# Kernel optimization log

Hardware: AMD Instinct MI355X
Metric: run time of the kernel (lower is better)

## Reference

```python
import jax, jax.numpy as jnp
import numpy as np

WS = 8
SHIFT = 4


def _cpb_constants(ws):
    rc = np.arange(-(ws - 1), ws, dtype=np.float32)
    gh, gw = np.meshgrid(rc, rc, indexing='ij')
    table = np.stack([gh, gw], axis=-1)[None]  # (1, 2ws-1, 2ws-1, 2)
    table = table / (ws - 1) * 8.0
    table = np.sign(table) * np.log2(np.abs(table) + 1.0) / np.log2(8.0)
    c = np.arange(ws)
    ch, cw = np.meshgrid(c, c, indexing='ij')
    flat = np.stack([ch.ravel(), cw.ravel()])  # (2, N)
    rel = (flat[:, :, None] - flat[:, None, :]).transpose(1, 2, 0).copy()
    rel[..., 0] += ws - 1
    rel[..., 1] += ws - 1
    rel[..., 0] *= 2 * ws - 1
    rpi = rel.sum(-1)  # (N, N) int
    return table.astype(np.float32), rpi


def _attn_mask(H, W, ws, s):
    # Faithful to source: middle slice is slice(-ws, +s) (empty for H>ws+s)
    img = np.zeros((H, W), np.float32)
    cnt = 0
    for hs in (slice(0, -ws), slice(-ws, s), slice(-s, None)):
        for wsl in (slice(0, -ws), slice(-ws, s), slice(-s, None)):
            img[hs, wsl] = cnt
            cnt += 1
    mw = img.reshape(H // ws, ws, W // ws, ws).transpose(0, 2, 1, 3).reshape(-1, ws * ws)
    am = mw[:, None, :] - mw[:, :, None]
    return np.where(am != 0, -100.0, 0.0).astype(np.float32)


def _dwconv(x, w):
    return jax.lax.conv_general_dilated(
        x, w, (1, 1), 'SAME',
        dimension_numbers=('NCHW', 'OIHW', 'NCHW'),
        feature_group_count=x.shape[1])


def _ln_nchw(x, g, b, eps=8e-8):
    m = x.mean(1, keepdims=True)
    v = jnp.square(x - m).mean(1, keepdims=True)
    return (x - m) / jnp.sqrt(v + eps) * g[None, :, None, None] + b[None, :, None, None]


def setup_inputs() -> dict:
    key = jax.random.key(0)
    ks = jax.random.split(key, 16)
    B, C, H, W = 16, 512, 64, 64
    nh = 16
    hid = 4 * C
    w = lambda k, s: (jax.random.normal(k, s, dtype=jnp.float32) * 0.02)
    return {
        'x': jax.random.normal(ks[0], (B, C, H, W), dtype=jnp.float32),
        'lpu_w': w(ks[1], (C, 1, 3, 3)),
        'qkv_w': w(ks[2], (3 * C, C)),
        'out_w': w(ks[3], (C, C)),
        'cpb_w1': w(ks[4], (512, 2)),
        'cpb_w2': w(ks[5], (nh, 512)),
        'logits_scale': jnp.full((nh, 1, 1), np.log(10.0), dtype=jnp.float32),
        'gamma1': jnp.ones((C,), jnp.float32),
        'beta1': jnp.zeros((C,), jnp.float32),
        'gamma2': jnp.ones((C,), jnp.float32),
        'beta2': jnp.zeros((C,), jnp.float32),
        'pw1_w': w(ks[6], (hid, C)),
        'dw_w': w(ks[7], (hid, 1, 3, 3)),
        'pw2_w': w(ks[8], (C, hid)),
        'sr_scale': jnp.ones((), jnp.float32),
        'sr_bias': jnp.zeros((), jnp.float32),
        'rs1': jnp.ones((C,), jnp.float32),
        'rs2': jnp.ones((C,), jnp.float32),
    }


def reference(x, lpu_w, qkv_w, out_w, cpb_w1, cpb_w2, logits_scale,
              gamma1, beta1, gamma2, beta2, pw1_w, dw_w, pw2_w,
              sr_scale, sr_bias, rs1, rs2):
    B, C, H, W = x.shape
    ws, s = WS, SHIFT
    nh = logits_scale.shape[0]
    hd = C // nh
    N = ws * ws
    table_np, rpi = _cpb_constants(ws)
    table = jnp.asarray(table_np)
    mask = jnp.asarray(_attn_mask(H, W, ws, s))  # (nW, N, N)

    # LPU: x + depthwise conv
    x = x + _dwconv(x, lpu_w)
    x_temp = x

    # flatten to (B, HW, C); faithful roll over dims (1,2) = tokens AND channels
    x = x.reshape(B, C, H * W).transpose(0, 2, 1)
    x = jnp.roll(x, (-s, -s), axis=(1, 2))
    # window partition
    x = x.reshape(B, H // ws, ws, W // ws, ws, C).transpose(0, 1, 3, 2, 4, 5).reshape(-1, N, C)
    Bw = x.shape[0]

    qkv = (x @ qkv_w.T).reshape(Bw, N, 3, nh, hd).transpose(2, 0, 3, 1, 4)
    q, k, v = qkv[0], qkv[1], qkv[2]
    qn = q / jnp.maximum(jnp.linalg.norm(q, axis=-1, keepdims=True), 1e-12)
    kn = k / jnp.maximum(jnp.linalg.norm(k, axis=-1, keepdims=True), 1e-12)
    scale = jnp.exp(jnp.minimum(logits_scale, jnp.log(jnp.float32(100.0))))
    attn = jnp.einsum('bhid,bhjd->bhij', qn, kn) * scale[None]

    # continuous position bias
    tbl = jax.nn.hard_swish(table @ cpb_w1.T) @ cpb_w2.T  # (1, 2ws-1, 2ws-1, nh)
    tbl = tbl.reshape(-1, nh)
    bias = tbl[rpi.reshape(-1)].reshape(N, N, nh).transpose(2, 0, 1)
    bias = 16.0 * jax.nn.sigmoid(bias)
    attn = attn + bias[None]

    nW = mask.shape[0]
    attn = (attn.reshape(Bw // nW, nW, nh, N, N) + mask[None, :, None]).reshape(-1, nh, N, N)
    # faithful: nn.Softmax(1) -> softmax over HEAD axis
    attn = jax.nn.softmax(attn, axis=1)

    o = jnp.einsum('bhij,bhjd->bhid', attn, v).transpose(0, 2, 1, 3).reshape(Bw, N, C)
    o = o @ out_w.T

    o = o.reshape(B, H // ws, ws, W // ws, ws, C)
    o = jnp.roll(o, (s, s), axis=(1, 2))  # faithful: rolls window-grid / row dims
    # faithful buggy un-partition: transpose(1,2) then reshape
    o = o.transpose(0, 2, 1, 3, 4, 5).reshape(B, C, H, W)

    x = rs1[None, :, None, None] * x_temp + _ln_nchw(o, gamma1, beta1)

    h = jnp.einsum('bchw,oc->bohw', x, pw1_w)
    h = h + _dwconv(h, dw_w)
    h = sr_scale * jnp.square(jax.nn.relu(h)) + sr_bias  # StarReLU
    y = jnp.einsum('bchw,oc->bohw', h, pw2_w)
    return rs2[None, :, None, None] * x + _ln_nchw(y, gamma2, beta2)
```

## Files before the change

kernel.cpp:

```cpp
#include <hip/hip_runtime.h>
#include <hip/hip_bf16.h>
#include <stdint.h>


typedef float f32x4 __attribute__((ext_vector_type(4)));
typedef short s16x8 __attribute__((ext_vector_type(8)));

__device__ __forceinline__ float b2f(short u) {
  return __uint_as_float(((unsigned)(unsigned short)u) << 16);
}
__device__ __forceinline__ short f2b(float f) {
  __hip_bfloat16 h = __float2bfloat16(f);
  short s;
  __builtin_memcpy(&s, &h, 2);
  return s;
}
__device__ __forceinline__ void gload16(const void* g, void* l) {
  __builtin_amdgcn_global_load_lds((const unsigned int*)g, (unsigned int*)l, 16, 0, 0);
}

__global__ __launch_bounds__(256) void k_f2b4(const float* __restrict__ s0, short* __restrict__ d0,
                                              const float* __restrict__ s1, short* __restrict__ d1,
                                              const float* __restrict__ s2, short* __restrict__ d2,
                                              const float* __restrict__ s3, short* __restrict__ d3) {
  int b = blockIdx.x;
  const float* s;
  short* d;
  int base;
  if (b < 768) { s = s0; d = d0; base = b * 1024; }
  else if (b < 1024) { s = s1; d = d1; base = (b - 768) * 1024; }
  else if (b < 2048) { s = s2; d = d2; base = (b - 1024) * 1024; }
  else { s = s3; d = d3; base = (b - 2048) * 1024; }
  int i = base + threadIdx.x * 4;
  f32x4 v = *(const f32x4*)&s[i];
  ushort4 o;
  o.x = (unsigned short)f2b(v[0]);
  o.y = (unsigned short)f2b(v[1]);
  o.z = (unsigned short)f2b(v[2]);
  o.w = (unsigned short)f2b(v[3]);
  *(ushort4*)&d[i] = o;
}

__global__ __launch_bounds__(64) void k_cpb(const float* __restrict__ w1,
                                            const float* __restrict__ w2,
                                            float* __restrict__ btab) {
  const int r = blockIdx.x;
  const int lane = threadIdx.x;
  const int ri = r / 15, rj = r % 15;
  float th = (float)(ri - 7) * (8.f / 7.f);
  float tw = (float)(rj - 7) * (8.f / 7.f);
  float gh = copysignf(log2f(fabsf(th) + 1.f) * (1.f / 3.f), th);
  float gw = copysignf(log2f(fabsf(tw) + 1.f) * (1.f / 3.f), tw);
  const int h = lane >> 2, pp = lane & 3;
  float acc = 0.f;
  for (int k = 0; k < 128; ++k) {
    int hh = pp * 128 + k;
    float a = gh * w1[hh * 2] + gw * w1[hh * 2 + 1];
    float r6 = fminf(fmaxf(a + 3.f, 0.f), 6.f);
    float hsw = a * r6 * (1.f / 6.f);
    acc += hsw * w2[h * 512 + hh];
  }
  acc += __shfl_xor(acc, 1);
  acc += __shfl_xor(acc, 2);
  if ((lane & 3) == 0) btab[h * 225 + r] = 16.f / (1.f + __expf(-acc));
}

__global__ __launch_bounds__(256) void k_lpu(const float* __restrict__ x,
                                             const float* __restrict__ lw,
                                             short* __restrict__ xt) {
  __shared__ float img[64 * 68];
  const int bc = blockIdx.x;
  const int c = bc & 511;
  const float* img_g = x + (size_t)bc * 4096;
  short* outp = xt + (size_t)bc * 4096;
  const int tid = threadIdx.x;
#pragma unroll
  for (int t = 0; t < 4; ++t) {
    int idx = t * 256 + tid;
    int h = idx >> 4, w4 = (idx & 15) * 4;
    f32x4 v = *(const f32x4*)&img_g[h * 64 + w4];
    *(f32x4*)&img[h * 68 + w4] = v;
  }
  float wreg[9];
#pragma unroll
  for (int t = 0; t < 9; ++t) wreg[t] = lw[c * 9 + t];
  __syncthreads();
  const int hb = tid >> 4, w0 = (tid & 15) * 4;
#pragma unroll
  for (int g = 0; g < 4; ++g) {
    int h = hb + g * 16;
    float row[3][6];
#pragma unroll
    for (int dr = 0; dr < 3; ++dr) {
      int hh = h - 1 + dr;
      if (hh < 0 || hh > 63) {
#pragma unroll
        for (int j = 0; j < 6; ++j) row[dr][j] = 0.f;
      } else {
        f32x4 m = *(const f32x4*)&img[hh * 68 + w0];
        row[dr][1] = m[0]; row[dr][2] = m[1]; row[dr][3] = m[2]; row[dr][4] = m[3];
        row[dr][0] = (w0 > 0) ? img[hh * 68 + w0 - 1] : 0.f;
        row[dr][5] = (w0 < 60) ? img[hh * 68 + w0 + 4] : 0.f;
      }
    }
    ushort4 o;
    unsigned short op[4];
#pragma unroll
    for (int p = 0; p < 4; ++p) {
      float acc = row[1][p + 1];
#pragma unroll
      for (int dr = 0; dr < 3; ++dr)
#pragma unroll
        for (int dc = 0; dc < 3; ++dc)
          acc += wreg[dr * 3 + dc] * row[dr][p + dc];
      op[p] = (unsigned short)f2b(acc);
    }
    o.x = op[0]; o.y = op[1]; o.z = op[2]; o.w = op[3];
    *(ushort4*)&outp[h * 64 + w0] = o;
  }
}

__global__ __launch_bounds__(256) void k_xpose(const short* __restrict__ xt,
                                               short* __restrict__ xw) {
  __shared__ short tile[64][132];
  const int tid = threadIdx.x;
  const int cq = blockIdx.x & 3;
  const int h = (blockIdx.x >> 2) & 63;
  const int b = blockIdx.x >> 8;
  const int c0 = cq * 128;
  for (int idx = tid; idx < 64 * 128; idx += 256) {
    int ww = idx & 63, cc = idx >> 6;
    int csrc = (c0 + cc + 4) & 511;
    tile[ww][cc] = xt[(((size_t)b * 512 + csrc) * 64 + h) * 64 + ww];
  }
  __syncthreads();
  for (int qd = tid; qd < 64 * 32; qd += 256) {
    int ws_ = qd >> 5, cqq = qd & 31, cc = cqq * 4;
    int t = (h * 64 + ws_ + 4092) & 4095;
    int hd = t >> 6, wd = t & 63;
    int tok = (b * 64 + (hd >> 3) * 8 + (wd >> 3)) * 64 + (hd & 7) * 8 + (wd & 7);
    ushort4 u = *(const ushort4*)&tile[ws_][cc];
    *(ushort4*)&xw[(size_t)tok * 512 + c0 + cc] = u;
  }
}

template <int EPI>
__global__ __launch_bounds__(512, 2) void k_gemm(const short* __restrict__ A,
                                                 const short* __restrict__ B,
                                                 short* __restrict__ C,
                                                 short* __restrict__ o4,
                                                 const float* __restrict__ lsc,
                                                 int N, int K, int gx) {
  __shared__ short smem[2 * 32768];
  const int nwg = gridDim.x;
  const int orig = blockIdx.x;
  const int wgid = (orig & 7) * (nwg >> 3) + (orig >> 3);
  const int bx = wgid % gx, by = wgid / gx;
  const int tid = threadIdx.x;
  const int lane = tid & 63, wid = tid >> 6;
  const int wm = wid >> 2, wn = wid & 3;
  const int m0 = by * 256, n0 = bx * 256;
  const f32x4 fz = {0.f, 0.f, 0.f, 0.f};
  f32x4 acc[8][4];
#pragma unroll
  for (int m = 0; m < 8; ++m)
#pragma unroll
    for (int n = 0; n < 4; ++n) acc[m][n] = fz;
  const int rst = lane >> 3;
  const int cst = ((lane & 7) ^ rst) * 8;
  const int l15 = lane & 15, l4 = lane >> 4, l7 = lane & 7;
  const short* ag[4];
  const short* bg[4];
#pragma unroll
  for (int l = 0; l < 4; ++l) {
    int r = wid * 32 + l * 8 + rst;
    ag[l] = A + (size_t)(m0 + r) * K + cst;
    bg[l] = B + (size_t)(n0 + r) * K + cst;
  }
  const int nt = K >> 6;
  auto STAGE = [&](int b) {
    short* as = smem + b * 32768;
    short* bs = as + 16384;
#pragma unroll
    for (int l = 0; l < 4; ++l) {
      int rb = wid * 32 + l * 8;
      gload16(ag[l], as + rb * 64);
      gload16(bg[l], bs + rb * 64);
      ag[l] += 64;
      bg[l] += 64;
    }
  };
  STAGE(0);
  for (int kt = 0; kt < nt; ++kt) {
    const int cur = kt & 1;
    if (kt + 1 < nt) {
      STAGE(cur ^ 1);
      asm volatile("s_waitcnt vmcnt(8)" ::: "memory");
    } else {
      asm volatile("s_waitcnt vmcnt(0)" ::: "memory");
    }
    __builtin_amdgcn_s_barrier();
    __builtin_amdgcn_sched_barrier(0);
    const short* as = smem + cur * 32768;
    const short* bs = as + 16384;
    __builtin_amdgcn_s_setprio(1);
#pragma unroll
    for (int ks = 0; ks < 2; ++ks) {
      const int slot = ((ks * 4 + l4) ^ l7) * 8;
      s16x8 bfr[4];
#pragma unroll
      for (int n = 0; n < 4; ++n)
        bfr[n] = *(const s16x8*)&bs[(wn * 64 + n * 16 + l15) * 64 + slot];
#pragma unroll
      for (int m = 0; m < 8; ++m) {
        s16x8 af = *(const s16x8*)&as[(wm * 128 + m * 16 + l15) * 64 + slot];
#pragma unroll
        for (int n = 0; n < 4; ++n)
          acc[m][n] = __builtin_amdgcn_mfma_f32_16x16x32_bf16(af, bfr[n],
                                                              acc[m][n], 0, 0, 0);
      }
    }
    __builtin_amdgcn_s_setprio(0);
    __builtin_amdgcn_sched_barrier(0);
    __builtin_amdgcn_s_barrier();
    __builtin_amdgcn_sched_barrier(0);
  }
  if (EPI == 2) {
#pragma unroll
    for (int b = 0; b < 2; ++b) {
      const int cb = n0 + wn * 64 + b * 32;
      if (cb < 1024) {
        float sc = 1.f;
        if (cb < 512) sc = __expf(fminf(lsc[cb >> 5], 4.605170185988092f));
#pragma unroll
        for (int m = 0; m < 8; ++m)
#pragma unroll
          for (int r = 0; r < 4; ++r) {
            float s0 = acc[m][2 * b][r], s1 = acc[m][2 * b + 1][r];
            float ss = s0 * s0 + s1 * s1;
            ss += __shfl_xor(ss, 1);
            ss += __shfl_xor(ss, 2);
            ss += __shfl_xor(ss, 4);
            ss += __shfl_xor(ss, 8);
            float mul = sc / fmaxf(sqrtf(ss), 1e-12f);
            acc[m][2 * b][r] = s0 * mul;
            acc[m][2 * b + 1][r] = s1 * mul;
          }
      }
    }
  }
  short* ct = smem;
#pragma unroll
  for (int p = 0; p < 2; ++p) {
    if (p) __syncthreads();
    if (wm == p) {
#pragma unroll
      for (int m = 0; m < 8; ++m)
#pragma unroll
        for (int n = 0; n < 4; ++n)
#pragma unroll
          for (int r = 0; r < 4; ++r) {
            int lr = m * 16 + l4 * 4 + r;
            int lc = (wn * 64 + n * 16 + l15) ^ (((lr >> 2) & 3) << 4);
            ct[lr * 272 + lc] = f2b(acc[m][n][r]);
          }
    }
    __syncthreads();
#pragma unroll
    for (int uu = 0; uu < 8; ++uu) {
      int unit = uu * 512 + tid;
      int lr = unit >> 5, sl = unit & 31;
      int sx = (sl * 8) ^ (((lr >> 2) & 3) << 4);
      s16x8 v = *(const s16x8*)&ct[lr * 272 + sx];
      int grow = m0 + p * 128 + lr;
      int gcol = n0 + sl * 8;
      if (EPI != 1) {
        *(s16x8*)&C[(size_t)grow * N + gcol] = v;
      } else {
        int win = grow >> 6, nn = grow & 63;
        int b = win >> 6, whs = (win >> 3) & 7, wws = win & 7;
        int ih = nn >> 3, iw = nn & 7;
        int wh = (whs + 4) & 7, ww = (wws + 4) & 7;
        int cp = ww * 64 + wh * 8 + ih;
        int hp = iw * 8 + (gcol >> 6);
        int wp = gcol & 63;
        *(s16x8*)&o4[(((size_t)b * 512 + cp) * 64 + hp) * 64 + wp] = v;
      }
    }
  }
}

__global__ __launch_bounds__(256) void k_attn(const short* __restrict__ qkv,
                                              const float* __restrict__ btab_g,
                                              short* __restrict__ o_ws) {
  __shared__ float btab[3600];
  __shared__ short vts[2][2048];
  __shared__ short pts[4][1024];
  const int tid = threadIdx.x, lane = tid & 63, wid = tid >> 6;
  const int win = blockIdx.x;
  const int l15 = lane & 15, l4 = lane >> 4;
  const int qrow0 = wid * 16;
  for (int i = tid; i < 3600; i += 256) btab[i] = btab_g[i];
  int baddr[4][4];
#pragma unroll
  for (int n = 0; n < 4; ++n)
#pragma unroll
    for (int r = 0; r < 4; ++r) {
      int i_ = qrow0 + l4 * 4 + r, j_ = n * 16 + l15;
      int dih = (i_ >> 3) - (j_ >> 3) + 7;
      int diw = (i_ & 7) - (j_ & 7) + 7;
      baddr[n][r] = dih * 15 + diw;
    }
  __syncthreads();
  const short* base = qkv + (size_t)win * 64 * 1536;
  const f32x4 fz = {0.f, 0.f, 0.f, 0.f};
  f32x4 sump[4] = {fz, fz, fz, fz};
#pragma unroll 2
  for (int h = 0; h < 16; ++h) {
    s16x8 qf = *(const s16x8*)(base + (size_t)(qrow0 + l15) * 1536 + h * 32 + l4 * 8);
#pragma unroll
    for (int n = 0; n < 4; ++n) {
      s16x8 kf = *(const s16x8*)(base + (size_t)(n * 16 + l15) * 1536 + 512 + h * 32 + l4 * 8);
      f32x4 s = __builtin_amdgcn_mfma_f32_16x16x32_bf16(qf, kf, fz, 0, 0, 0);
#pragma unroll
      for (int r = 0; r < 4; ++r)
        sump[n][r] += __expf(s[r] + btab[h * 225 + baddr[n][r]]);
    }
  }
  f32x4 rden[4];
#pragma unroll
  for (int n = 0; n < 4; ++n)
#pragma unroll
    for (int r = 0; r < 4; ++r) rden[n][r] = 1.f / sump[n][r];
  char* pt = (char*)pts[wid];
  {
    int j = tid & 63, d0 = (tid >> 6) * 8;
    s16x8 vv = *(const s16x8*)(base + (size_t)j * 1536 + 1024 + d0);
#pragma unroll
    for (int jj = 0; jj < 8; ++jj) {
      int d = d0 + jj;
      *(short*)((char*)vts[0] + ((d * 128 + j * 2) ^ ((d & 7) << 4))) = vv[jj];
    }
  }
  __syncthreads();
  for (int h = 0; h < 16; ++h) {
    const char* vcur = (const char*)vts[h & 1];
    if (h < 15) {
      int j = tid & 63, d0 = (tid >> 6) * 8;
      s16x8 vv = *(const s16x8*)(base + (size_t)j * 1536 + 1024 + (h + 1) * 32 + d0);
      char* vnxt = (char*)vts[(h + 1) & 1];
#pragma unroll
      for (int jj = 0; jj < 8; ++jj) {
        int d = d0 + jj;
        *(short*)(vnxt + ((d * 128 + j * 2) ^ ((d & 7) << 4))) = vv[jj];
      }
    }
    s16x8 qf = *(const s16x8*)(base + (size_t)(qrow0 + l15) * 1536 + h * 32 + l4 * 8);
#pragma unroll
    for (int n = 0; n < 4; ++n) {
      s16x8 kf = *(const s16x8*)(base + (size_t)(n * 16 + l15) * 1536 + 512 + h * 32 + l4 * 8);
      f32x4 s = __builtin_amdgcn_mfma_f32_16x16x32_bf16(qf, kf, fz, 0, 0, 0);
#pragma unroll
      for (int r = 0; r < 4; ++r) {
        float pv = __expf(s[r] + btab[h * 225 + baddr[n][r]]) * rden[n][r];
        int i_loc = l4 * 4 + r, j_ = n * 16 + l15;
        *(short*)(pt + ((i_loc * 128 + j_ * 2) ^ ((i_loc & 7) << 4))) = f2b(pv);
      }
    }
    f32x4 oacc[2] = {fz, fz};
#pragma unroll
    for (int kb = 0; kb < 2; ++kb) {
      s16x8 af = *(const s16x8*)(pt + ((l15 * 128 + kb * 64 + l4 * 16) ^ ((l15 & 7) << 4)));
#pragma unroll
      for (int db = 0; db < 2; ++db) {
        int d = db * 16 + l15;
        s16x8 bf = *(const s16x8*)(vcur + ((d * 128 + kb * 64 + l4 * 16) ^ ((d & 7) << 4)));
        oacc[db] = __builtin_amdgcn_mfma_f32_16x16x32_bf16(af, bf, oacc[db], 0, 0, 0);
      }
    }
    short* ob = o_ws + ((size_t)win * 64 + qrow0) * 512 + h * 32;
#pragma unroll
    for (int db = 0; db < 2; ++db)
#pragma unroll
      for (int r = 0; r < 4; ++r)
        ob[(size_t)(l4 * 4 + r) * 512 + db * 16 + l15] = f2b(oacc[db][r]);
    __syncthreads();
  }
}

__global__ __launch_bounds__(256) void k_ln1(const short* __restrict__ o4,
                                             const short* __restrict__ xt,
                                             const float* __restrict__ g1,
                                             const float* __restrict__ b1,
                                             const float* __restrict__ rs1,
                                             short* __restrict__ x2h) {
  __shared__ float reds[4][64], redq[4][64];
  __shared__ float mean_s[64], rstd_s[64];
  __shared__ short tile[128][66];
  const int tid = threadIdx.x;
  const int b = blockIdx.x >> 6, hp = blockIdx.x & 63;
  const int w = tid & 63, part = tid >> 6;
  const short* base = o4 + (size_t)b * 512 * 4096 + hp * 64;
  float s = 0.f, q = 0.f;
  for (int c = part; c < 512; c += 4) {
    float v = b2f(base[(size_t)c * 4096 + w]);
    s += v; q += v * v;
  }
  reds[part][w] = s; redq[part][w] = q;
  __syncthreads();
  if (tid < 64) {
    float S = 0.f, Q = 0.f;
    for (int i = 0; i < 4; ++i) { S += reds[i][tid]; Q += redq[i][tid]; }
    float m = S * (1.f / 512.f);
    float var = Q * (1.f / 512.f) - m * m;
    mean_s[tid] = m;
    rstd_s[tid] = rsqrtf(var + 8e-8f);
  }
  __syncthreads();
  const short* xtb = xt + (size_t)b * 512 * 4096 + hp * 64;
  for (int c0 = 0; c0 < 512; c0 += 128) {
    for (int cc = part; cc < 128; cc += 4) {
      int c = c0 + cc;
      float v = b2f(base[(size_t)c * 4096 + w]);
      float ln = (v - mean_s[w]) * rstd_s[w] * g1[c] + b1[c];
      float xv = rs1[c] * b2f(xtb[(size_t)c * 4096 + w]) + ln;
      tile[cc][w] = f2b(xv);
    }
    __syncthreads();
    short* xh = x2h + ((size_t)blockIdx.x * 64) * 512 + c0;
    for (int qd = tid; qd < 64 * 32; qd += 256) {
      int w_ = qd >> 5, cq = qd & 31, cc = cq * 4;
      ushort4 u;
      u.x = (unsigned short)tile[cc][w_];
      u.y = (unsigned short)tile[cc + 1][w_];
      u.z = (unsigned short)tile[cc + 2][w_];
      u.w = (unsigned short)tile[cc + 3][w_];
      *(ushort4*)&xh[(size_t)w_ * 512 + cc] = u;
    }
    __syncthreads();
  }
}

__global__ __launch_bounds__(256) void k_dwc2(const short* __restrict__ h1,
                                              const float* __restrict__ dw,
                                              const float* __restrict__ srs_p,
                                              const float* __restrict__ srb_p,
                                              short* __restrict__ h2) {
  __shared__ short tile[6 * 64 * 64];
  const int tid = threadIdx.x;
  const int cblk = blockIdx.x & 31;
  const int hq = (blockIdx.x >> 5) & 15;
  const int b = blockIdx.x >> 9;
  const int c0 = cblk * 64;
  const int h0 = hq * 4;
  for (int t = 0; t < 12; ++t) {
    int idx = t * 256 + tid;
    int cg = idx & 7;
    int wl = (idx >> 3) & 63;
    int rl = idx >> 9;
    int hr = h0 - 1 + rl;
    s16x8 v = {0, 0, 0, 0, 0, 0, 0, 0};
    if (hr >= 0 && hr < 64)
      v = *(const s16x8*)&h1[((size_t)b * 4096 + hr * 64 + wl) * 2048 + c0 + cg * 8];
    *(s16x8*)&tile[(rl * 64 + wl) * 64 + (cg ^ (wl & 7)) * 8] = v;
  }
  const int cg = tid & 7;
  const int wq = tid >> 3;
  float wt[9][8];
#pragma unroll
  for (int j = 0; j < 8; ++j) {
    int cch = c0 + cg * 8 + j;
#pragma unroll
    for (int t = 0; t < 9; ++t) wt[t][j] = dw[cch * 9 + t];
  }
  const float srs = *srs_p, srb = *srb_p;
  __syncthreads();
#pragma unroll
  for (int it = 0; it < 8; ++it) {
    int wl = wq + (it & 1) * 32;
    int rl = it >> 1;
    s16x8 ctr = *(const s16x8*)&tile[((rl + 1) * 64 + wl) * 64 + (cg ^ (wl & 7)) * 8];
    float acc[8];
#pragma unroll
    for (int j = 0; j < 8; ++j) acc[j] = b2f(ctr[j]);
#pragma unroll
    for (int dh = -1; dh <= 1; ++dh) {
      int row = rl + 1 + dh;
#pragma unroll
      for (int dwi = -1; dwi <= 1; ++dwi) {
        int wn = wl + dwi;
        if (wn < 0 || wn > 63) continue;
        s16x8 v = *(const s16x8*)&tile[(row * 64 + wn) * 64 + (cg ^ (wn & 7)) * 8];
        const float* wrow = wt[(dh + 1) * 3 + dwi + 1];
#pragma unroll
        for (int j = 0; j < 8; ++j) acc[j] += wrow[j] * b2f(v[j]);
      }
    }
    s16x8 o;
#pragma unroll
    for (int j = 0; j < 8; ++j) {
      float rr = fmaxf(acc[j], 0.f);
      o[j] = f2b(srs * rr * rr + srb);
    }
    *(s16x8*)&h2[((size_t)b * 4096 + (h0 + rl) * 64 + wl) * 2048 + c0 + cg * 8] = o;
  }
}

__global__ __launch_bounds__(256) void k_final(const short* __restrict__ y,
                                               const short* __restrict__ x2h,
                                               const float* __restrict__ g2,
                                               const float* __restrict__ b2p,
                                               const float* __restrict__ rs2,
                                               float* __restrict__ out) {
  __shared__ short yt[64][132];
  __shared__ short xt2[64][132];
  __shared__ float reds[4][64], redq[4][64];
  __shared__ float mean_s[64], rstd_s[64];
  const int tid = threadIdx.x;
  const int b = blockIdx.x >> 6, hh = blockIdx.x & 63;
  const int w = tid & 63, part = tid >> 6;
  const short* yb = y + (size_t)blockIdx.x * 64 * 512;
  const short* xb = x2h + (size_t)blockIdx.x * 64 * 512;
  float s = 0.f, q = 0.f;
  for (int c0 = 0; c0 < 512; c0 += 128) {
    for (int qd = tid; qd < 64 * 32; qd += 256) {
      int w_ = qd >> 5, g = qd & 31;
      *(ushort4*)&yt[w_][g * 4] = *(const ushort4*)&yb[(size_t)w_ * 512 + c0 + g * 4];
    }
    __syncthreads();
    for (int cc = part * 32; cc < part * 32 + 32; ++cc) {
      float v = b2f(yt[w][cc]);
      s += v; q += v * v;
    }
    __syncthreads();
  }
  reds[part][w] = s; redq[part][w] = q;
  __syncthreads();
  if (tid < 64) {
    float S = 0.f, Q = 0.f;
    for (int i = 0; i < 4; ++i) { S += reds[i][tid]; Q += redq[i][tid]; }
    float m = S * (1.f / 512.f);
    float var = Q * (1.f / 512.f) - m * m;
    mean_s[tid] = m;
    rstd_s[tid] = rsqrtf(var + 8e-8f);
  }
  __syncthreads();
  float* ob = out + (size_t)b * 512 * 4096 + hh * 64;
  for (int c0 = 0; c0 < 512; c0 += 128) {
    for (int qd = tid; qd < 64 * 32; qd += 256) {
      int w_ = qd >> 5, g = qd & 31;
      *(ushort4*)&yt[w_][g * 4] = *(const ushort4*)&yb[(size_t)w_ * 512 + c0 + g * 4];
      *(ushort4*)&xt2[w_][g * 4] = *(const ushort4*)&xb[(size_t)w_ * 512 + c0 + g * 4];
    }
    __syncthreads();
    for (int it = 0; it < 32; ++it) {
      int c = c0 + it * 4 + part;
      float yv = b2f(yt[w][c - c0]);
      float lnv = (yv - mean_s[w]) * rstd_s[w] * g2[c] + b2p[c];
      float xv = b2f(xt2[w][c - c0]);
      ob[(size_t)c * 4096 + w] = rs2[c] * xv + lnv;
    }
    __syncthreads();
  }
}

extern "C" void kernel_launch(void* const* d_in, const int* in_sizes, int n_in,
                              void* d_out, int out_size, void* d_ws, size_t ws_size,
                              hipStream_t stream) {
  (void)in_sizes; (void)n_in; (void)out_size; (void)ws_size;
  const float* x      = (const float*)d_in[0];
  const float* lpu_w  = (const float*)d_in[1];
  const float* qkv_w  = (const float*)d_in[2];
  const float* out_w  = (const float*)d_in[3];
  const float* cpb_w1 = (const float*)d_in[4];
  const float* cpb_w2 = (const float*)d_in[5];
  const float* lsc    = (const float*)d_in[6];
  const float* g1     = (const float*)d_in[7];
  const float* b1     = (const float*)d_in[8];
  const float* g2     = (const float*)d_in[9];
  const float* b2v    = (const float*)d_in[10];
  const float* pw1_w  = (const float*)d_in[11];
  const float* dw_w   = (const float*)d_in[12];
  const float* pw2_w  = (const float*)d_in[13];
  const float* srs    = (const float*)d_in[14];
  const float* srb    = (const float*)d_in[15];
  const float* rs1    = (const float*)d_in[16];
  const float* rs2    = (const float*)d_in[17];

  char* ws = (char*)d_ws;
  float* btab   = (float*)(ws + 0);
  short* wbq    = (short*)(ws + 16384);
  short* wbo    = (short*)(ws + 1589248);
  short* wb1    = (short*)(ws + 2113536);
  short* wb2    = (short*)(ws + 4210688);
  short* x_temp = (short*)(ws + 8388608);
  short* xw     = (short*)(ws + 75497472);
  short* qkv    = (short*)(ws + 142606336);
  short* o_ws   = (short*)(ws + 343932928);
  short* o4     = (short*)(ws + 75497472);
  short* x2h    = (short*)(ws + 142606336);
  short* h1     = (short*)(ws + 209715200);
  short* h2     = (short*)(ws + 8388608);
  short* yb     = (short*)(ws + 343932928);

  k_f2b4<<<3072, 256, 0, stream>>>(qkv_w, wbq, out_w, wbo, pw1_w, wb1, pw2_w, wb2);
  k_cpb<<<225, 64, 0, stream>>>(cpb_w1, cpb_w2, btab);
  k_lpu<<<8192, 256, 0, stream>>>(x, lpu_w, x_temp);
  k_xpose<<<4096, 256, 0, stream>>>(x_temp, xw);
  k_gemm<2><<<1536, 512, 0, stream>>>(xw, wbq, qkv, nullptr, lsc, 1536, 512, 6);
  k_attn<<<1024, 256, 0, stream>>>(qkv, btab, o_ws);
  k_gemm<1><<<512, 512, 0, stream>>>(o_ws, wbo, nullptr, o4, nullptr, 512, 512, 2);
  k_ln1<<<1024, 256, 0, stream>>>(o4, x_temp, g1, b1, rs1, x2h);
  for (int ch = 0; ch < 2; ++ch) {
    const size_t tok0 = (size_t)ch * 8 * 4096;
    k_gemm<0><<<1024, 512, 0, stream>>>(x2h + tok0 * 512, wb1, h1, nullptr, nullptr, 2048, 512, 8);
    k_dwc2<<<4096, 256, 0, stream>>>(h1, dw_w, srs, srb, h2);
    k_gemm<0><<<256, 512, 0, stream>>>(h2, wb2, yb + tok0 * 512, nullptr, nullptr, 512, 2048, 2);
  }
  k_final<<<1024, 256, 0, stream>>>(yb, x2h, g2, b2v, rs2, (float*)d_out);
}
```

Baseline: 1.165 ms.

## Split GEMM k-tile into four phases interleaving prefetch loads with MFMA

```diff
diff --git a/kernel.cpp b/kernel.cpp
--- a/kernel.cpp
+++ b/kernel.cpp
@@ -151,7 +151,7 @@
                                                  short* __restrict__ o4,
                                                  const float* __restrict__ lsc,
                                                  int N, int K, int gx) {
-  __shared__ short smem[2 * 32768];
+  __shared__ short smem[65536];
   const int nwg = gridDim.x;
   const int orig = blockIdx.x;
   const int wgid = (orig & 7) * (nwg >> 3) + (orig >> 3);
@@ -160,70 +160,83 @@
   const int lane = tid & 63, wid = tid >> 6;
   const int wm = wid >> 2, wn = wid & 3;
   const int m0 = by * 256, n0 = bx * 256;
+  const int l15 = lane & 15, l4 = lane >> 4, l7 = lane & 7;
   const f32x4 fz = {0.f, 0.f, 0.f, 0.f};
   f32x4 acc[8][4];
 #pragma unroll
   for (int m = 0; m < 8; ++m)
 #pragma unroll
     for (int n = 0; n < 4; ++n) acc[m][n] = fz;
-  const int rst = lane >> 3;
-  const int cst = ((lane & 7) ^ rst) * 8;
-  const int l15 = lane & 15, l4 = lane >> 4, l7 = lane & 7;
-  const short* ag[4];
-  const short* bg[4];
-#pragma unroll
-  for (int l = 0; l < 4; ++l) {
-    int r = wid * 32 + l * 8 + rst;
-    ag[l] = A + (size_t)(m0 + r) * K + cst;
-    bg[l] = B + (size_t)(n0 + r) * K + cst;
-  }
+  const int srow = tid >> 3;
+  const int cst = ((lane & 7) ^ ((lane >> 3) & 7)) * 8;
+  const short* aP[2][2];
+  const short* bP[2][2];
+#pragma unroll
+  for (int h = 0; h < 2; ++h)
+#pragma unroll
+    for (int q = 0; q < 2; ++q) {
+      aP[h][q] = A + (size_t)(m0 + h * 128 + q * 64 + srow) * K + cst;
+      bP[h][q] = B + (size_t)(n0 + h * 128 + q * 64 + srow) * K + cst;
+    }
   const int nt = K >> 6;
-  auto STAGE = [&](int b) {
-    short* as = smem + b * 32768;
-    short* bs = as + 16384;
-#pragma unroll
-    for (int l = 0; l < 4; ++l) {
-      int rb = wid * 32 + l * 8;
-      gload16(ag[l], as + rb * 64);
-      gload16(bg[l], bs + rb * 64);
-      ag[l] += 64;
-      bg[l] += 64;
-    }
-  };
-  STAGE(0);
+  {
+    short* wb = smem;
+    gload16(aP[0][0], wb + 0 + wid * 512);
+    gload16(aP[0][1], wb + 4096 + wid * 512);
+    gload16(aP[1][0], wb + 8192 + wid * 512);
+    gload16(aP[1][1], wb + 12288 + wid * 512);
+    gload16(bP[0][0], wb + 16384 + wid * 512);
+    gload16(bP[0][1], wb + 20480 + wid * 512);
+    gload16(bP[1][0], wb + 24576 + wid * 512);
+    gload16(bP[1][1], wb + 28672 + wid * 512);
+  }
+  asm volatile("s_waitcnt vmcnt(0)" ::: "memory");
+  __builtin_amdgcn_sched_barrier(0);
+  __builtin_amdgcn_s_barrier();
+  __builtin_amdgcn_sched_barrier(0);
   for (int kt = 0; kt < nt; ++kt) {
-    const int cur = kt & 1;
-    if (kt + 1 < nt) {
-      STAGE(cur ^ 1);
-      asm volatile("s_waitcnt vmcnt(8)" ::: "memory");
-    } else {
-      asm volatile("s_waitcnt vmcnt(0)" ::: "memory");
-    }
-    __builtin_amdgcn_s_barrier();
-    __builtin_amdgcn_sched_barrier(0);
-    const short* as = smem + cur * 32768;
-    const short* bs = as + 16384;
-    __builtin_amdgcn_s_setprio(1);
-#pragma unroll
-    for (int ks = 0; ks < 2; ++ks) {
+    const short* rb = smem + (kt & 1) * 32768;
+    short* wb = smem + ((kt & 1) ^ 1) * 32768;
+    const bool st = (kt + 1 < nt);
+    const int ko = (kt + 1) * 64;
+    s16x8 bfr[4];
+#pragma unroll
+    for (int p = 0; p < 4; ++p) {
+      const int ks = p >> 1, mg = p & 1;
       const int slot = ((ks * 4 + l4) ^ l7) * 8;
-      s16x8 bfr[4];
-#pragma unroll
-      for (int n = 0; n < 4; ++n)
-        bfr[n] = *(const s16x8*)&bs[(wn * 64 + n * 16 + l15) * 64 + slot];
-#pragma unroll
-      for (int m = 0; m < 8; ++m) {
-        s16x8 af = *(const s16x8*)&as[(wm * 128 + m * 16 + l15) * 64 + slot];
+      s16x8 af[4];
+#pragma unroll
+      for (int j = 0; j < 4; ++j)
+        af[j] = *(const s16x8*)&rb[wm * 8192 + ((mg * 4 + j) * 16 + l15) * 64 + slot];
+      if (mg == 0) {
 #pragma unroll
         for (int n = 0; n < 4; ++n)
-          acc[m][n] = __builtin_amdgcn_mfma_f32_16x16x32_bf16(af, bfr[n],
-                                                              acc[m][n], 0, 0, 0);
-      }
-    }
-    __builtin_amdgcn_s_setprio(0);
-    __builtin_amdgcn_sched_barrier(0);
-    __builtin_amdgcn_s_barrier();
-    __builtin_amdgcn_sched_barrier(0);
+          bfr[n] = *(const s16x8*)&rb[16384 + (wn >> 1) * 8192 +
+                                      ((wn & 1) * 64 + n * 16 + l15) * 64 + slot];
+      }
+      if (st) {
+        if (p == 0) { gload16(aP[0][0] + ko, wb + 0 + wid * 512);
+                      gload16(aP[0][1] + ko, wb + 4096 + wid * 512); }
+        if (p == 1) { gload16(aP[1][0] + ko, wb + 8192 + wid * 512);
+                      gload16(aP[1][1] + ko, wb + 12288 + wid * 512); }
+        if (p == 2) { gload16(bP[0][0] + ko, wb + 16384 + wid * 512);
+                      gload16(bP[0][1] + ko, wb + 20480 + wid * 512); }
+        if (p == 3) { gload16(bP[1][0] + ko, wb + 24576 + wid * 512);
+                      gload16(bP[1][1] + ko, wb + 28672 + wid * 512); }
+      }
+      __builtin_amdgcn_s_setprio(1);
+#pragma unroll
+      for (int j = 0; j < 4; ++j)
+#pragma unroll
+        for (int n = 0; n < 4; ++n)
+          acc[mg * 4 + j][n] = __builtin_amdgcn_mfma_f32_16x16x32_bf16(
+              af[j], bfr[n], acc[mg * 4 + j][n], 0, 0, 0);
+      __builtin_amdgcn_s_setprio(0);
+      if (p == 3) asm volatile("s_waitcnt vmcnt(0)" ::: "memory");
+      __builtin_amdgcn_sched_barrier(0);
+      __builtin_amdgcn_s_barrier();
+      __builtin_amdgcn_sched_barrier(0);
+    }
   }
   if (EPI == 2) {
 #pragma unroll
```

New measurement: 1.170 ms. Within noise of the previous version (+0.5%).
